# Kernel tuning notes

Measured on AMD Instinct MI355X. Metric: run time of the kernel, lower is better.

The kernel has to match this reference:

```python
import jax, jax.numpy as jnp
import numpy as np

K = 20  # neighbors per point (module default)


def _knn_idx(x, k):
    # x: [N, d] -> indices of k nearest points (self included, as in torch_cluster.knn)
    d2 = jnp.sum(x * x, axis=-1)
    dist = d2[:, None] + d2[None, :] - 2.0 * (x @ x.T)  # [N, N] squared distances
    _, idx = jax.lax.top_k(-dist, k)  # smallest distances
    return idx  # [N, k]


def _mlp(h, layers):
    # layers: list of (W, b, relu_flag); BN is identity (eval mode, fresh running stats)
    for W, b, relu in layers:
        h = h @ W + b
        if relu:
            h = jax.nn.relu(h)
    return h


def _dynamic_edge_conv(x, layers, k=K):
    # x: [B, N, d]; dynamic kNN graph per graph, edge feat [x_i, x_j - x_i], MLP, max-aggr
    idx = jax.vmap(lambda xx: _knn_idx(jax.lax.stop_gradient(xx), k))(x)  # [B, N, k]
    xj = jax.vmap(lambda xx, ii: xx[ii])(x, idx)  # [B, N, k, d] neighbor gather
    xi = x[:, :, None, :]
    feat = jnp.concatenate([jnp.broadcast_to(xi, xj.shape), xj - xi], axis=-1)  # [B,N,k,2d]
    return jnp.max(_mlp(feat, layers), axis=2)  # [B, N, d_out]


def setup_inputs() -> dict:
    key = jax.random.key(0)
    ks = jax.random.split(key, 20)
    s = 0.05
    B, N, PD, OUT = 8, 4096, 2, 10
    f32 = jnp.float32

    def w(k, shape):
        return jax.random.normal(k, shape, dtype=f32) * s

    return {
        "data": jax.random.normal(ks[0], (B, N, PD), dtype=f32),
        # conv1 MLP: [2*PD, 64, 64, 64]
        "c1w1": w(ks[1], (2 * PD, 64)), "c1b1": jnp.zeros((64,), f32),
        "c1w2": w(ks[2], (64, 64)),     "c1b2": jnp.zeros((64,), f32),
        "c1w3": w(ks[3], (64, 64)),     "c1b3": jnp.zeros((64,), f32),
        # conv2 MLP: [2*64, 128]
        "c2w1": w(ks[4], (128, 128)),   "c2b1": jnp.zeros((128,), f32),
        # lin1: 192 -> 1024
        "lin1_w": w(ks[5], (192, 1024)), "lin1_b": jnp.zeros((1024,), f32),
        # head MLP: [1024, 512, 256, OUT]
        "mw1": w(ks[6], (1024, 512)), "mb1": jnp.zeros((512,), f32),
        "mw2": w(ks[7], (512, 256)),  "mb2": jnp.zeros((256,), f32),
        "mw3": w(ks[8], (256, OUT)),  "mb3": jnp.zeros((OUT,), f32),
    }


def reference(data, c1w1, c1b1, c1w2, c1b2, c1w3, c1b3, c2w1, c2b1,
              lin1_w, lin1_b, mw1, mb1, mw2, mb2, mw3, mb3):
    # DynamicEdgeConv 1: MLP([4,64,64,64]) (plain last layer)
    x1 = _dynamic_edge_conv(data, [(c1w1, c1b1, True), (c1w2, c1b2, True), (c1w3, c1b3, False)])
    # DynamicEdgeConv 2: MLP([128,128]) (single plain linear)
    x2 = _dynamic_edge_conv(x1, [(c2w1, c2b1, False)])
    out = jnp.concatenate([x1, x2], axis=-1) @ lin1_w + lin1_b  # [B, N, 1024]
    out = jnp.max(out, axis=1)  # global max pool over points -> [B, 1024]
    out = _mlp(out, [(mw1, mb1, True), (mw2, mb2, True), (mw3, mb3, False)])
    return jax.nn.log_softmax(out, axis=1)
```

## Files before the change

### kernel.cpp

```cpp
#include <hip/hip_runtime.h>
#include <math.h>

#define DEVI static __device__ __forceinline__
#define F_INF __builtin_inff()

typedef short bf16x8 __attribute__((ext_vector_type(8)));
typedef float floatx4 __attribute__((ext_vector_type(4)));
typedef unsigned short ub16x4 __attribute__((ext_vector_type(4)));

DEVI unsigned short bf16rne(float f)
{
    unsigned u = __float_as_uint(f);
    unsigned r = (u + 0x7FFFu + ((u >> 16) & 1u)) >> 16;
    return (unsigned short)r;
}
DEVI float bf16tof(unsigned short h) { return __uint_as_float(((unsigned)h) << 16); }

DEVI bool lexlt(float d, int i, float dr, int ir)
{
    return (d < dr) || (d == dr && i < ir);
}

DEVI void insert20(float* bd, int* bi, float d, int i)
{
#pragma unroll
    for (int j = 19; j >= 1; --j) {
        bool lt  = d < bd[j];
        bool ltp = d < bd[j - 1];
        float nd = ltp ? bd[j - 1] : d;
        int   ni = ltp ? bi[j - 1] : i;
        bd[j] = lt ? nd : bd[j];
        bi[j] = lt ? ni : bi[j];
    }
    bool lt0 = d < bd[0];
    bd[0] = lt0 ? d : bd[0];
    bi[0] = lt0 ? i : bi[0];
}

DEVI void insert_tiered(float* bd, int* bi, float d, int i)
{
    if (__all(!(d < bd[15]))) {
#pragma unroll
        for (int j = 19; j >= 17; --j) {
            bool lt  = d < bd[j];
            bool ltp = d < bd[j - 1];
            float nd = ltp ? bd[j - 1] : d;
            int   ni = ltp ? bi[j - 1] : i;
            bd[j] = lt ? nd : bd[j];
            bi[j] = lt ? ni : bi[j];
        }
        bool lt16 = d < bd[16];
        bd[16] = lt16 ? d : bd[16];
        bi[16] = lt16 ? i : bi[16];
    } else if (__all(!(d < bd[7]))) {
#pragma unroll
        for (int j = 19; j >= 9; --j) {
            bool lt  = d < bd[j];
            bool ltp = d < bd[j - 1];
            float nd = ltp ? bd[j - 1] : d;
            int   ni = ltp ? bi[j - 1] : i;
            bd[j] = lt ? nd : bd[j];
            bi[j] = lt ? ni : bi[j];
        }
        bool lt8 = d < bd[8];
        bd[8] = lt8 ? d : bd[8];
        bi[8] = lt8 ? i : bi[8];
    } else {
        insert20(bd, bi, d, i);
    }
}

DEVI void flushT(float* bd, int* bi, float d, int i, int e, int cnt)
{
    bool want = (e < cnt) && (d < bd[19]);
    if (__any(want))
        insert_tiered(bd, bi, want ? d : F_INF, want ? i : 0x7FFFFFFF);
}

#define FLUSH() do { \
    flushT(bd, bi, a0, j0, 0, cnt); \
    flushT(bd, bi, a1, j1, 1, cnt); \
    flushT(bd, bi, a2, j2, 2, cnt); \
    flushT(bd, bi, a3, j3, 3, cnt); \
    cnt = 0; thr = bd[19]; \
} while (0)

#define APPEND(dv, civ) do { \
    bool pass_ = (dv) < thr; \
    if (pass_) { \
        a0 = (cnt == 0) ? (dv) : a0; j0 = (cnt == 0) ? (civ) : j0; \
        a1 = (cnt == 1) ? (dv) : a1; j1 = (cnt == 1) ? (civ) : j1; \
        a2 = (cnt == 2) ? (dv) : a2; j2 = (cnt == 2) ? (civ) : j2; \
        a3 = (cnt == 3) ? (dv) : a3; j3 = (cnt == 3) ? (civ) : j3; \
        ++cnt; \
    } \
    if (__any(cnt == 4)) { FLUSH(); } \
} while (0)

__global__ __launch_bounds__(64) void k_merge8(const float* __restrict__ partD,
                                               const int* __restrict__ partI,
                                               int* __restrict__ idxo)
{
    int q = blockIdx.x * 64 + threadIdx.x;
    const float* rd = partD + (size_t)q * 160;
    const int*   ri = partI + (size_t)q * 160;
    int p0 = 0, p1 = 0, p2 = 0, p3 = 0, p4 = 0, p5 = 0, p6 = 0, p7 = 0;
    int* op = idxo + (size_t)q * 20;
    for (int r = 0; r < 20; ++r) {
        float d0 = rd[p0],        d1 = rd[20 + p1];
        float d2v = rd[40 + p2],  d3 = rd[60 + p3];
        float d4 = rd[80 + p4],   d5 = rd[100 + p5];
        float d6 = rd[120 + p6],  d7 = rd[140 + p7];
        int   i0 = ri[p0],        i1 = ri[20 + p1];
        int   i2 = ri[40 + p2],   i3 = ri[60 + p3];
        int   i4v = ri[80 + p4],  i5 = ri[100 + p5];
        int   i6 = ri[120 + p6],  i7 = ri[140 + p7];
        bool wA = lexlt(d1, i1, d0, i0);   float dA = wA ? d1 : d0; int iA = wA ? i1 : i0; int sA = wA ? 1 : 0;
        bool wB = lexlt(d3, i3, d2v, i2);  float dB = wB ? d3 : d2v; int iB = wB ? i3 : i2; int sB = wB ? 3 : 2;
        bool wC = lexlt(d5, i5, d4, i4v);  float dC = wC ? d5 : d4; int iC = wC ? i5 : i4v; int sC = wC ? 5 : 4;
        bool wD = lexlt(d7, i7, d6, i6);   float dD = wD ? d7 : d6; int iD = wD ? i7 : i6; int sD = wD ? 7 : 6;
        bool wE = lexlt(dB, iB, dA, iA);   float dE = wE ? dB : dA; int iE = wE ? iB : iA; int sE = wE ? sB : sA;
        bool wF = lexlt(dD, iD, dC, iC);   float dF = wF ? dD : dC; int iF = wF ? iD : iC; int sF = wF ? sD : sC;
        bool wG = lexlt(dF, iF, dE, iE);   int ig = wG ? iF : iE;   int sg = wG ? sF : sE;
        op[r] = ig;
        p0 += (sg == 0); p1 += (sg == 1); p2 += (sg == 2); p3 += (sg == 3);
        p4 += (sg == 4); p5 += (sg == 5); p6 += (sg == 6); p7 += (sg == 7);
    }
}

__global__ __launch_bounds__(256, 4) void k_knn2d(const float* __restrict__ x,
                                                  float* __restrict__ partD, int* __restrict__ partI)
{
    __shared__ float2 pts[4096];
    int t = threadIdx.x;
    int blk = blockIdx.x;
    int b = blk >> 7;
    int qt = (blk >> 1) & 63;
    int s = blk & 1;
    const float* xb = x + (size_t)b * 4096 * 2;
    for (int f = t; f < 2048; f += 256)
        ((float4*)pts)[f] = ((const float4*)xb)[f];
    __syncthreads();

    int l = t & 63, w = t >> 6;
    int q = qt * 64 + l;
    float2 qp = pts[q];
    float d2i = qp.x * qp.x + qp.y * qp.y;

    float bd[20]; int bi[20];
#pragma unroll
    for (int j = 0; j < 20; ++j) { bd[j] = F_INF; bi[j] = -1; }
    int cnt = 0; float thr = F_INF;
    float a0 = 0, a1 = 0, a2 = 0, a3 = 0;
    int   j0 = 0, j1 = 0, j2 = 0, j3 = 0;

    int m0 = s * 2048 + w * 512;
    for (int m = m0; m < m0 + 512; ++m) {
        float2 p = pts[m];
        float d2j = p.x * p.x + p.y * p.y;
        float dot = qp.x * p.x + qp.y * p.y;
        float dist = (d2i + d2j) - 2.0f * dot;
        APPEND(dist, m);
    }
    FLUSH();

    size_t base = (((size_t)(b * 4096 + q)) * 8 + s * 4 + w) * 20;
#pragma unroll
    for (int k = 0; k < 20; ++k) { partD[base + k] = bd[k]; partI[base + k] = bi[k]; }
}

__global__ void k_prep1(const float* __restrict__ x, const float* __restrict__ w1,
                        const float* __restrict__ b1, float* __restrict__ pm, float* __restrict__ qv)
{
    int tid = blockIdx.x * 256 + threadIdx.x;
    int n = tid >> 6, i = tid & 63;
    float x0 = x[(size_t)n * 2], x1v = x[(size_t)n * 2 + 1];
    float wa = w1[i], wb = w1[64 + i], wc = w1[128 + i], wd = w1[192 + i];
    pm[tid] = fmaf(x0, wa - wc, fmaf(x1v, wb - wd, b1[i]));
    qv[tid] = fmaf(x0, wc, x1v * wd);
}

__global__ __launch_bounds__(256) void k_edge1(const float* __restrict__ pm, const float* __restrict__ q,
                                               const int* __restrict__ idx1,
                                               const float* __restrict__ w2, const float* __restrict__ b2,
                                               const float* __restrict__ w3, const float* __restrict__ b3,
                                               float* __restrict__ x1, float* __restrict__ d2x1)
{
    int t = threadIdx.x;
    int w = t >> 6, l = t & 63;
    int pg = l / 20;
    int k  = l - pg * 20;
    int n0 = blockIdx.x * 12 + w * 3 + pg;
    bool valid = (l < 60) && (n0 < 32768);
    int n = valid ? n0 : 0;
    int b = n >> 12;
    int j = idx1[(size_t)n * 20 + k];
    const float4* pmr = (const float4*)(pm + (size_t)n * 64);
    const float4* qr  = (const float4*)(q + ((size_t)(b * 4096) + j) * 64);

    float h1[64];
#pragma unroll
    for (int i4 = 0; i4 < 16; ++i4) {
        float4 a = pmr[i4], c = qr[i4];
        h1[i4 * 4 + 0] = fmaxf(a.x + c.x, 0.f);
        h1[i4 * 4 + 1] = fmaxf(a.y + c.y, 0.f);
        h1[i4 * 4 + 2] = fmaxf(a.z + c.z, 0.f);
        h1[i4 * 4 + 3] = fmaxf(a.w + c.w, 0.f);
    }
    float h2[64];
#pragma unroll
    for (int o = 0; o < 64; ++o) h2[o] = b2[o];
#pragma unroll
    for (int i = 0; i < 64; ++i) {
        const float* r = w2 + i * 64;
#pragma unroll
        for (int o = 0; o < 64; ++o) h2[o] = fmaf(h1[i], r[o], h2[o]);
    }
#pragma unroll
    for (int o = 0; o < 64; ++o) h2[o] = fmaxf(h2[o], 0.f);

    float h3[64];
#pragma unroll
    for (int o = 0; o < 64; ++o) h3[o] = b3[o];
#pragma unroll
    for (int i = 0; i < 64; ++i) {
        const float* r = w3 + i * 64;
#pragma unroll
        for (int o = 0; o < 64; ++o) h3[o] = fmaf(h2[i], r[o], h3[o]);
    }

    int s16 = (k + 16 < 20) ? (l + 16) : l;
    int s8  = (k + 8  < 20) ? (l + 8)  : l;
    int s4  = (k + 4  < 20) ? (l + 4)  : l;
    int s2  = (k + 2  < 20) ? (l + 2)  : l;
    int s1  = (k + 1  < 20) ? (l + 1)  : l;
#pragma unroll
    for (int o = 0; o < 64; ++o) {
        float v = h3[o];
        v = fmaxf(v, __shfl(v, s16));
        v = fmaxf(v, __shfl(v, s8));
        v = fmaxf(v, __shfl(v, s4));
        v = fmaxf(v, __shfl(v, s2));
        v = fmaxf(v, __shfl(v, s1));
        h3[o] = v;
    }
    if (valid && k == 0) {
        float d2 = 0.f;
#pragma unroll
        for (int o = 0; o < 64; ++o) d2 += h3[o] * h3[o];
        float4* op = (float4*)(x1 + (size_t)n * 64);
#pragma unroll
        for (int i4 = 0; i4 < 16; ++i4)
            op[i4] = make_float4(h3[i4 * 4], h3[i4 * 4 + 1], h3[i4 * 4 + 2], h3[i4 * 4 + 3]);
        d2x1[n] = d2;
    }
}

__global__ __launch_bounds__(256) void k_split(const float* __restrict__ x1,
                                               unsigned short* __restrict__ xh,
                                               unsigned short* __restrict__ xm,
                                               unsigned short* __restrict__ xl)
{
    int id = blockIdx.x * 256 + threadIdx.x;
    float4 v = ((const float4*)x1)[id];
    float vv[4] = { v.x, v.y, v.z, v.w };
    ub16x4 h, m, l;
#pragma unroll
    for (int i = 0; i < 4; ++i) {
        float x = vv[i];
        unsigned short hb = bf16rne(x);  float fh = bf16tof(hb);
        float r1 = x - fh;
        unsigned short mb = bf16rne(r1); float fm = bf16tof(mb);
        float r2 = r1 - fm;
        unsigned short lb = bf16rne(r2);
        h[i] = hb; m[i] = mb; l[i] = lb;
    }
    ((ub16x4*)xh)[id] = h;
    ((ub16x4*)xm)[id] = m;
    ((ub16x4*)xl)[id] = l;
}

__global__ __launch_bounds__(256, 3) void k_knn64(const unsigned short* __restrict__ xh,
                                                  const unsigned short* __restrict__ xm,
                                                  const unsigned short* __restrict__ xl,
                                                  const float* __restrict__ d2x1,
                                                  float* __restrict__ partD, int* __restrict__ partI)
{
    __shared__ unsigned short qlds[1536 * 8];
    __shared__ float dlds[4 * 16 * 68];
    __shared__ float d2cL[64];

    int t = threadIdx.x;
    int blk = blockIdx.x;
    int bb = blk >> 7;
    int qt = (blk >> 1) & 63;
    int s  = blk & 1;
    int qbase  = bb * 4096 + qt * 64;
    int cstart = s * 2048;
    int w = t >> 6, l = t & 63;
    int r16 = l & 15, g = l >> 4;

    {
        const unsigned short* pp[3] = { xh, xm, xl };
        for (int f = t; f < 1536; f += 256) {
            int lane = f & 63, kc = (f >> 6) & 1, qb = (f >> 7) & 3, pl = f >> 9;
            size_t off = ((size_t)(qbase + qb * 16 + (lane & 15))) * 64 + kc * 32 + 8 * (lane >> 4);
            ((bf16x8*)qlds)[f] = *(const bf16x8*)(pp[pl] + off);
        }
    }
    float d2ql = d2x1[qbase + l];
    __syncthreads();

    float bd[20]; int bi[20];
#pragma unroll
    for (int j = 0; j < 20; ++j) { bd[j] = F_INF; bi[j] = -1; }
    int cnt = 0; float thr = F_INF;
    float a0 = 0, a1 = 0, a2 = 0, a3 = 0;
    int   j0 = 0, j1 = 0, j2 = 0, j3 = 0;

    const bf16x8* qf = (const bf16x8*)qlds;
    float* myD = dlds + w * 16 * 68;

    for (int T = 0; T < 32; ++T) {
        int csl = cstart + T * 64 + 16 * w;
        int csg = bb * 4096 + csl;

        bf16x8 bh[2], bm[2], blv[2];
#pragma unroll
        for (int kc = 0; kc < 2; ++kc) {
            size_t off = ((size_t)(csg + r16)) * 64 + kc * 32 + 8 * g;
            bh[kc]  = *(const bf16x8*)(xh + off);
            bm[kc]  = *(const bf16x8*)(xm + off);
            blv[kc] = *(const bf16x8*)(xl + off);
        }
        if (l < 16) d2cL[w * 16 + l] = d2x1[csg + l];

        floatx4 acc[4];
#pragma unroll
        for (int qb = 0; qb < 4; ++qb) acc[qb] = (floatx4){0.f, 0.f, 0.f, 0.f};
#pragma unroll
        for (int qb = 0; qb < 4; ++qb)
#pragma unroll
            for (int kc = 0; kc < 2; ++kc) {
                bf16x8 qh_ = qf[((0 * 4 + qb) * 2 + kc) * 64 + l];
                bf16x8 qm_ = qf[((1 * 4 + qb) * 2 + kc) * 64 + l];
                bf16x8 ql_ = qf[((2 * 4 + qb) * 2 + kc) * 64 + l];
                acc[qb] = __builtin_amdgcn_mfma_f32_16x16x32_bf16(qh_, bh[kc],  acc[qb], 0, 0, 0);
                acc[qb] = __builtin_amdgcn_mfma_f32_16x16x32_bf16(qh_, bm[kc],  acc[qb], 0, 0, 0);
                acc[qb] = __builtin_amdgcn_mfma_f32_16x16x32_bf16(qm_, bh[kc],  acc[qb], 0, 0, 0);
                acc[qb] = __builtin_amdgcn_mfma_f32_16x16x32_bf16(qm_, bm[kc],  acc[qb], 0, 0, 0);
                acc[qb] = __builtin_amdgcn_mfma_f32_16x16x32_bf16(qh_, blv[kc], acc[qb], 0, 0, 0);
                acc[qb] = __builtin_amdgcn_mfma_f32_16x16x32_bf16(ql_, bh[kc],  acc[qb], 0, 0, 0);
            }

#pragma unroll
        for (int qb = 0; qb < 4; ++qb)
#pragma unroll
            for (int rr = 0; rr < 4; ++rr)
                myD[r16 * 68 + qb * 16 + g * 4 + rr] = acc[qb][rr];

#pragma unroll
        for (int c = 0; c < 16; ++c) {
            float dot = myD[c * 68 + l];
            float dist = (d2ql + d2cL[w * 16 + c]) - 2.0f * dot;
            APPEND(dist, csl + c);
        }
    }
    FLUSH();

    size_t base = (((size_t)(qbase + l)) * 8 + s * 4 + w) * 20;
#pragma unroll
    for (int k = 0; k < 20; ++k) { partD[base + k] = bd[k]; partI[base + k] = bi[k]; }
}

__global__ __launch_bounds__(128) void k_prep2(const float* __restrict__ x1, const float* __restrict__ w,
                                               const float* __restrict__ bias,
                                               float* __restrict__ T, float* __restrict__ V)
{
    __shared__ float xs[8][64];
    int o = threadIdx.x;
    int g = blockIdx.x * 8;
    for (int t = threadIdx.x; t < 512; t += 128) xs[t >> 6][t & 63] = x1[(size_t)g * 64 + t];
    __syncthreads();
    float at[8] = {}, av[8] = {};
    for (int i = 0; i < 64; ++i) {
        float wt = w[i * 128 + o], wv = w[(64 + i) * 128 + o];
#pragma unroll
        for (int p = 0; p < 8; ++p) {
            float xv = xs[p][i];
            at[p] = fmaf(xv, wt, at[p]);
            av[p] = fmaf(xv, wv, av[p]);
        }
    }
    float bo = bias[o];
#pragma unroll
    for (int p = 0; p < 8; ++p) {
        T[(size_t)(g + p) * 128 + o] = at[p] - av[p] + bo;
        V[(size_t)(g + p) * 128 + o] = av[p];
    }
}

__global__ __launch_bounds__(256) void k_edge2(const float* __restrict__ T, const float* __restrict__ V,
                                               const int* __restrict__ idx2, float* __restrict__ x2)
{
    int t = threadIdx.x;
    int p = t >> 5, oc = t & 31;
    int n = blockIdx.x * 8 + p;
    int b = n >> 12;
    const int* ip = idx2 + (size_t)n * 20;
    float4 mx = make_float4(-F_INF, -F_INF, -F_INF, -F_INF);
    for (int k = 0; k < 20; ++k) {
        int j = ip[k];
        float4 v = ((const float4*)(V + ((size_t)(b * 4096) + j) * 128))[oc];
        mx.x = fmaxf(mx.x, v.x); mx.y = fmaxf(mx.y, v.y);
        mx.z = fmaxf(mx.z, v.z); mx.w = fmaxf(mx.w, v.w);
    }
    float4 tv = ((const float4*)(T + (size_t)n * 128))[oc];
    float4 r = make_float4(tv.x + mx.x, tv.y + mx.y, tv.z + mx.z, tv.w + mx.w);
    ((float4*)(x2 + (size_t)n * 128))[oc] = r;
}

__global__ __launch_bounds__(256) void k_lin1max(const float* __restrict__ x1, const float* __restrict__ x2,
                                                 const float* __restrict__ w, const float* __restrict__ bias,
                                                 float* __restrict__ partial)
{
    __shared__ float fs[32][192];
    int blk = blockIdx.x;
    int b = blk >> 7, c = blk & 127;
    int base_n = b * 4096 + c * 32;
    for (int t = threadIdx.x; t < 2048; t += 256) {
        int n = t >> 6, i = t & 63;
        fs[n][i] = x1[(size_t)(base_n + n) * 64 + i];
    }
    for (int t = threadIdx.x; t < 4096; t += 256) {
        int n = t >> 7, i = t & 127;
        fs[n][64 + i] = x2[(size_t)(base_n + n) * 128 + i];
    }
    __syncthreads();

    float acc[32][4];
#pragma unroll
    for (int n = 0; n < 32; ++n)
#pragma unroll
        for (int oo = 0; oo < 4; ++oo) acc[n][oo] = 0.f;

    for (int i4 = 0; i4 < 48; ++i4) {
        float wv[4][4];
#pragma unroll
        for (int r = 0; r < 4; ++r)
#pragma unroll
            for (int oo = 0; oo < 4; ++oo)
                wv[r][oo] = w[(size_t)(i4 * 4 + r) * 1024 + oo * 256 + threadIdx.x];
#pragma unroll
        for (int n = 0; n < 32; ++n) {
            float4 f = *(const float4*)&fs[n][i4 * 4];
#pragma unroll
            for (int oo = 0; oo < 4; ++oo) {
                acc[n][oo] = fmaf(f.x, wv[0][oo], acc[n][oo]);
                acc[n][oo] = fmaf(f.y, wv[1][oo], acc[n][oo]);
                acc[n][oo] = fmaf(f.z, wv[2][oo], acc[n][oo]);
                acc[n][oo] = fmaf(f.w, wv[3][oo], acc[n][oo]);
            }
        }
    }
#pragma unroll
    for (int oo = 0; oo < 4; ++oo) {
        int o = oo * 256 + threadIdx.x;
        float m = -F_INF;
#pragma unroll
        for (int n = 0; n < 32; ++n) m = fmaxf(m, acc[n][oo]);
        partial[((size_t)b * 128 + c) * 1024 + o] = m + bias[o];
    }
}

__global__ void k_red(const float* __restrict__ partial, float* __restrict__ pooled)
{
    int t = blockIdx.x * 256 + threadIdx.x;
    int b = t >> 10, o = t & 1023;
    float m = -F_INF;
    for (int c = 0; c < 128; ++c) m = fmaxf(m, partial[((size_t)b * 128 + c) * 1024 + o]);
    pooled[t] = m;
}

__global__ __launch_bounds__(256) void k_fc1(const float* __restrict__ pooled, const float* __restrict__ w,
                                             const float* __restrict__ bias, float* __restrict__ g1)
{
    __shared__ float ps[8 * 1024];
    for (int t = threadIdx.x; t < 8192; t += 256) ps[t] = pooled[t];
    __syncthreads();
    int o = blockIdx.x * 256 + threadIdx.x;
    float acc[8] = {};
    for (int i4 = 0; i4 < 256; ++i4) {
        float w0 = w[(size_t)(i4 * 4 + 0) * 512 + o];
        float w1v = w[(size_t)(i4 * 4 + 1) * 512 + o];
        float w2v = w[(size_t)(i4 * 4 + 2) * 512 + o];
        float w3v = w[(size_t)(i4 * 4 + 3) * 512 + o];
#pragma unroll
        for (int bb = 0; bb < 8; ++bb) {
            float4 f = *(const float4*)&ps[bb * 1024 + i4 * 4];
            acc[bb] = fmaf(f.x, w0, fmaf(f.y, w1v, fmaf(f.z, w2v, fmaf(f.w, w3v, acc[bb]))));
        }
    }
    float bo = bias[o];
#pragma unroll
    for (int bb = 0; bb < 8; ++bb) g1[bb * 512 + o] = fmaxf(acc[bb] + bo, 0.f);
}

__global__ __launch_bounds__(256) void k_fc2(const float* __restrict__ g1, const float* __restrict__ w,
                                             const float* __restrict__ bias, float* __restrict__ g2)
{
    __shared__ float gs[8 * 512];
    for (int t = threadIdx.x; t < 4096; t += 256) gs[t] = g1[t];
    __syncthreads();
    int o = threadIdx.x;
    float acc[8] = {};
    for (int i4 = 0; i4 < 128; ++i4) {
        float w0 = w[(size_t)(i4 * 4 + 0) * 256 + o];
        float w1v = w[(size_t)(i4 * 4 + 1) * 256 + o];
        float w2v = w[(size_t)(i4 * 4 + 2) * 256 + o];
        float w3v = w[(size_t)(i4 * 4 + 3) * 256 + o];
#pragma unroll
        for (int bb = 0; bb < 8; ++bb) {
            float4 f = *(const float4*)&gs[bb * 512 + i4 * 4];
            acc[bb] = fmaf(f.x, w0, fmaf(f.y, w1v, fmaf(f.z, w2v, fmaf(f.w, w3v, acc[bb]))));
        }
    }
    float bo = bias[o];
#pragma unroll
    for (int bb = 0; bb < 8; ++bb) g2[bb * 256 + o] = fmaxf(acc[bb] + bo, 0.f);
}

__global__ void k_fc3sm(const float* __restrict__ g2, const float* __restrict__ w,
                        const float* __restrict__ bias, float* __restrict__ out)
{
    int t = threadIdx.x;
    int b = t >> 4, l = t & 15;
    float lg = -F_INF;
    if (l < 10) {
        float a = bias[l];
        for (int i = 0; i < 256; ++i) a = fmaf(g2[b * 256 + i], w[i * 10 + l], a);
        lg = a;
    }
    float m = lg;
    m = fmaxf(m, __shfl_xor(m, 1, 16));
    m = fmaxf(m, __shfl_xor(m, 2, 16));
    m = fmaxf(m, __shfl_xor(m, 4, 16));
    m = fmaxf(m, __shfl_xor(m, 8, 16));
    float e = (l < 10) ? expf(lg - m) : 0.f;
    float s = e;
    s += __shfl_xor(s, 1, 16);
    s += __shfl_xor(s, 2, 16);
    s += __shfl_xor(s, 4, 16);
    s += __shfl_xor(s, 8, 16);
    if (l < 10) out[b * 10 + l] = (lg - m) - logf(s);
}

extern "C" void kernel_launch(void* const* d_in, const int* in_sizes, int n_in,
                              void* d_out, int out_size, void* d_ws, size_t ws_size,
                              hipStream_t stream)
{
    (void)in_sizes; (void)n_in; (void)out_size; (void)ws_size;
    const float* data  = (const float*)d_in[0];
    const float* c1w1  = (const float*)d_in[1];
    const float* c1b1  = (const float*)d_in[2];
    const float* c1w2  = (const float*)d_in[3];
    const float* c1b2  = (const float*)d_in[4];
    const float* c1w3  = (const float*)d_in[5];
    const float* c1b3  = (const float*)d_in[6];
    const float* c2w1  = (const float*)d_in[7];
    const float* c2b1  = (const float*)d_in[8];
    const float* lin1w = (const float*)d_in[9];
    const float* lin1b = (const float*)d_in[10];
    const float* mw1   = (const float*)d_in[11];
    const float* mb1   = (const float*)d_in[12];
    const float* mw2   = (const float*)d_in[13];
    const float* mb2   = (const float*)d_in[14];
    const float* mw3   = (const float*)d_in[15];
    const float* mb3   = (const float*)d_in[16];
    float* ws  = (float*)d_ws;
    int*   wsi = (int*)d_ws;
    float* out = (float*)d_out;

    const size_t OFF_IDX1 = 0;
    const size_t OFF_IDX2 = 0;
    const size_t OFF_X1   = 655360;
    const size_t OFF_D2   = 2752512;
    const size_t OFF_PM   = 2785280;
    const size_t OFF_Q    = 4882432;
    const size_t OFF_PD   = 2785280;
    const size_t OFF_PI   = 8028160;
    const size_t OFF_T    = 2785280;
    const size_t OFF_V    = 6979584;
    const size_t OFF_X2   = 11173888;
    const size_t OFF_PART = 15368192;
    const size_t OFF_POOL = 16416768;
    const size_t OFF_G1   = 16424960;
    const size_t OFF_G2   = 16429056;
    const size_t OFF_XH   = 13271040;
    const size_t OFF_XM   = 14319616;
    const size_t OFF_XL   = 15368192;

    k_knn2d<<<1024, 256, 0, stream>>>(data, ws + OFF_PD, wsi + OFF_PI);
    k_merge8<<<512, 64, 0, stream>>>(ws + OFF_PD, wsi + OFF_PI, wsi + OFF_IDX1);
    k_prep1<<<8192, 256, 0, stream>>>(data, c1w1, c1b1, ws + OFF_PM, ws + OFF_Q);
    k_edge1<<<2731, 256, 0, stream>>>(ws + OFF_PM, ws + OFF_Q, wsi + OFF_IDX1,
                                      c1w2, c1b2, c1w3, c1b3, ws + OFF_X1, ws + OFF_D2);
    k_split<<<2048, 256, 0, stream>>>(ws + OFF_X1,
                                      (unsigned short*)(ws + OFF_XH),
                                      (unsigned short*)(ws + OFF_XM),
                                      (unsigned short*)(ws + OFF_XL));
    k_knn64<<<1024, 256, 0, stream>>>((const unsigned short*)(ws + OFF_XH),
                                      (const unsigned short*)(ws + OFF_XM),
                                      (const unsigned short*)(ws + OFF_XL),
                                      ws + OFF_D2, ws + OFF_PD, wsi + OFF_PI);
    k_merge8<<<512, 64, 0, stream>>>(ws + OFF_PD, wsi + OFF_PI, wsi + OFF_IDX2);
    k_prep2<<<4096, 128, 0, stream>>>(ws + OFF_X1, c2w1, c2b1, ws + OFF_T, ws + OFF_V);
    k_edge2<<<4096, 256, 0, stream>>>(ws + OFF_T, ws + OFF_V, wsi + OFF_IDX2, ws + OFF_X2);
    k_lin1max<<<1024, 256, 0, stream>>>(ws + OFF_X1, ws + OFF_X2, lin1w, lin1b, ws + OFF_PART);
    k_red<<<32, 256, 0, stream>>>(ws + OFF_PART, ws + OFF_POOL);
    k_fc1<<<2, 256, 0, stream>>>(ws + OFF_POOL, mw1, mb1, ws + OFF_G1);
    k_fc2<<<1, 256, 0, stream>>>(ws + OFF_G1, mw2, mb2, ws + OFF_G2);
    k_fc3sm<<<1, 128, 0, stream>>>(ws + OFF_G2, mw3, mb3, out);
}
```

Baseline: 1.663 ms.

## Interleave bf16 split planes, transpose partial top-k layout, reorder knn64 block mapping

Packs the three bf16 split planes (hi/mid/lo) of each point into one interleaved 192-element row, so each candidate's three fragments share cache lines. Changes the partial top-k buffers from per-query-contiguous to per-slice-major, so lanes in a wavefront write and read adjacent query records in the knn and merge kernels. Remaps k_knn64 block indices so consecutive blocks cover different batches with the same query tile, and adds a __syncthreads at the top of each candidate tile loop, which looks like a fix for an LDS reuse race. The extra barrier adds some synchronisation cost per tile.

```diff
diff --git a/kernel.cpp b/kernel.cpp
--- a/kernel.cpp
+++ b/kernel.cpp
@@ -101,20 +101,21 @@
                                                const int* __restrict__ partI,
                                                int* __restrict__ idxo)
 {
+    const size_t LS = 655360;
     int q = blockIdx.x * 64 + threadIdx.x;
-    const float* rd = partD + (size_t)q * 160;
-    const int*   ri = partI + (size_t)q * 160;
+    const float* rd = partD + (size_t)q * 20;
+    const int*   ri = partI + (size_t)q * 20;
     int p0 = 0, p1 = 0, p2 = 0, p3 = 0, p4 = 0, p5 = 0, p6 = 0, p7 = 0;
     int* op = idxo + (size_t)q * 20;
     for (int r = 0; r < 20; ++r) {
-        float d0 = rd[p0],        d1 = rd[20 + p1];
-        float d2v = rd[40 + p2],  d3 = rd[60 + p3];
-        float d4 = rd[80 + p4],   d5 = rd[100 + p5];
-        float d6 = rd[120 + p6],  d7 = rd[140 + p7];
-        int   i0 = ri[p0],        i1 = ri[20 + p1];
-        int   i2 = ri[40 + p2],   i3 = ri[60 + p3];
-        int   i4v = ri[80 + p4],  i5 = ri[100 + p5];
-        int   i6 = ri[120 + p6],  i7 = ri[140 + p7];
+        float d0 = rd[p0],            d1 = rd[LS + p1];
+        float d2v = rd[2 * LS + p2],  d3 = rd[3 * LS + p3];
+        float d4 = rd[4 * LS + p4],   d5 = rd[5 * LS + p5];
+        float d6 = rd[6 * LS + p6],   d7 = rd[7 * LS + p7];
+        int   i0 = ri[p0],            i1 = ri[LS + p1];
+        int   i2 = ri[2 * LS + p2],   i3 = ri[3 * LS + p3];
+        int   i4v = ri[4 * LS + p4],  i5 = ri[5 * LS + p5];
+        int   i6 = ri[6 * LS + p6],   i7 = ri[7 * LS + p7];
         bool wA = lexlt(d1, i1, d0, i0);   float dA = wA ? d1 : d0; int iA = wA ? i1 : i0; int sA = wA ? 1 : 0;
         bool wB = lexlt(d3, i3, d2v, i2);  float dB = wB ? d3 : d2v; int iB = wB ? i3 : i2; int sB = wB ? 3 : 2;
         bool wC = lexlt(d5, i5, d4, i4v);  float dC = wC ? d5 : d4; int iC = wC ? i5 : i4v; int sC = wC ? 5 : 4;
@@ -164,7 +165,7 @@
     }
     FLUSH();
 
-    size_t base = (((size_t)(b * 4096 + q)) * 8 + s * 4 + w) * 20;
+    size_t base = (((size_t)(s * 4 + w)) * 32768 + (b * 4096 + q)) * 20;
 #pragma unroll
     for (int k = 0; k < 20; ++k) { partD[base + k] = bd[k]; partI[base + k] = bi[k]; }
 }
@@ -257,11 +258,10 @@
 }
 
 __global__ __launch_bounds__(256) void k_split(const float* __restrict__ x1,
-                                               unsigned short* __restrict__ xh,
-                                               unsigned short* __restrict__ xm,
-                                               unsigned short* __restrict__ xl)
+                                               unsigned short* __restrict__ xi)
 {
     int id = blockIdx.x * 256 + threadIdx.x;
+    int n = id >> 4, dp = id & 15;
     float4 v = ((const float4*)x1)[id];
     float vv[4] = { v.x, v.y, v.z, v.w };
     ub16x4 h, m, l;
@@ -275,14 +275,13 @@
         unsigned short lb = bf16rne(r2);
         h[i] = hb; m[i] = mb; l[i] = lb;
     }
-    ((ub16x4*)xh)[id] = h;
-    ((ub16x4*)xm)[id] = m;
-    ((ub16x4*)xl)[id] = l;
-}
-
-__global__ __launch_bounds__(256, 3) void k_knn64(const unsigned short* __restrict__ xh,
-                                                  const unsigned short* __restrict__ xm,
-                                                  const unsigned short* __restrict__ xl,
+    size_t rb = (size_t)n * 192;
+    *(ub16x4*)(xi + rb +       dp * 4) = h;
+    *(ub16x4*)(xi + rb +  64 + dp * 4) = m;
+    *(ub16x4*)(xi + rb + 128 + dp * 4) = l;
+}
+
+__global__ __launch_bounds__(256, 3) void k_knn64(const unsigned short* __restrict__ xi,
                                                   const float* __restrict__ d2x1,
                                                   float* __restrict__ partD, int* __restrict__ partI)
 {
@@ -292,21 +291,19 @@
 
     int t = threadIdx.x;
     int blk = blockIdx.x;
-    int bb = blk >> 7;
-    int qt = (blk >> 1) & 63;
+    int qt = blk >> 4;
+    int bb = (blk >> 1) & 7;
     int s  = blk & 1;
     int qbase  = bb * 4096 + qt * 64;
     int cstart = s * 2048;
     int w = t >> 6, l = t & 63;
     int r16 = l & 15, g = l >> 4;
 
-    {
-        const unsigned short* pp[3] = { xh, xm, xl };
-        for (int f = t; f < 1536; f += 256) {
-            int lane = f & 63, kc = (f >> 6) & 1, qb = (f >> 7) & 3, pl = f >> 9;
-            size_t off = ((size_t)(qbase + qb * 16 + (lane & 15))) * 64 + kc * 32 + 8 * (lane >> 4);
-            ((bf16x8*)qlds)[f] = *(const bf16x8*)(pp[pl] + off);
-        }
+    for (int f = t; f < 1536; f += 256) {
+        int lane = f & 63, kc = (f >> 6) & 1, qb = (f >> 7) & 3, pl = f >> 9;
+        size_t off = ((size_t)(qbase + qb * 16 + (lane & 15))) * 192 + pl * 64
+                   + kc * 32 + 8 * (lane >> 4);
+        ((bf16x8*)qlds)[f] = *(const bf16x8*)(xi + off);
     }
     float d2ql = d2x1[qbase + l];
     __syncthreads();
@@ -322,16 +319,17 @@
     float* myD = dlds + w * 16 * 68;
 
     for (int T = 0; T < 32; ++T) {
+        __syncthreads();
         int csl = cstart + T * 64 + 16 * w;
         int csg = bb * 4096 + csl;
 
         bf16x8 bh[2], bm[2], blv[2];
 #pragma unroll
         for (int kc = 0; kc < 2; ++kc) {
-            size_t off = ((size_t)(csg + r16)) * 64 + kc * 32 + 8 * g;
-            bh[kc]  = *(const bf16x8*)(xh + off);
-            bm[kc]  = *(const bf16x8*)(xm + off);
-            blv[kc] = *(const bf16x8*)(xl + off);
+            size_t rb = ((size_t)(csg + r16)) * 192 + kc * 32 + 8 * g;
+            bh[kc]  = *(const bf16x8*)(xi + rb);
+            bm[kc]  = *(const bf16x8*)(xi + rb + 64);
+            blv[kc] = *(const bf16x8*)(xi + rb + 128);
         }
         if (l < 16) d2cL[w * 16 + l] = d2x1[csg + l];
 
@@ -368,7 +366,7 @@
     }
     FLUSH();
 
-    size_t base = (((size_t)(qbase + l)) * 8 + s * 4 + w) * 20;
+    size_t base = (((size_t)(s * 4 + w)) * 32768 + (qbase + l)) * 20;
 #pragma unroll
     for (int k = 0; k < 20; ++k) { partD[base + k] = bd[k]; partI[base + k] = bi[k]; }
 }
@@ -596,22 +594,15 @@
     const size_t OFF_POOL = 16416768;
     const size_t OFF_G1   = 16424960;
     const size_t OFF_G2   = 16429056;
-    const size_t OFF_XH   = 13271040;
-    const size_t OFF_XM   = 14319616;
-    const size_t OFF_XL   = 15368192;
+    const size_t OFF_XI   = 13271040;
 
     k_knn2d<<<1024, 256, 0, stream>>>(data, ws + OFF_PD, wsi + OFF_PI);
     k_merge8<<<512, 64, 0, stream>>>(ws + OFF_PD, wsi + OFF_PI, wsi + OFF_IDX1);
     k_prep1<<<8192, 256, 0, stream>>>(data, c1w1, c1b1, ws + OFF_PM, ws + OFF_Q);
     k_edge1<<<2731, 256, 0, stream>>>(ws + OFF_PM, ws + OFF_Q, wsi + OFF_IDX1,
                                       c1w2, c1b2, c1w3, c1b3, ws + OFF_X1, ws + OFF_D2);
-    k_split<<<2048, 256, 0, stream>>>(ws + OFF_X1,
-                                      (unsigned short*)(ws + OFF_XH),
-                                      (unsigned short*)(ws + OFF_XM),
-                                      (unsigned short*)(ws + OFF_XL));
-    k_knn64<<<1024, 256, 0, stream>>>((const unsigned short*)(ws + OFF_XH),
-                                      (const unsigned short*)(ws + OFF_XM),
-                                      (const unsigned short*)(ws + OFF_XL),
+    k_split<<<2048, 256, 0, stream>>>(ws + OFF_X1, (unsigned short*)(ws + OFF_XI));
+    k_knn64<<<1024, 256, 0, stream>>>((const unsigned short*)(ws + OFF_XI),
                                       ws + OFF_D2, ws + OFF_PD, wsi + OFF_PI);
     k_merge8<<<512, 64, 0, stream>>>(ws + OFF_PD, wsi + OFF_PI, wsi + OFF_IDX2);
     k_prep2<<<4096, 128, 0, stream>>>(ws + OFF_X1, c2w1, c2b1, ws + OFF_T, ws + OFF_V);
```

New measurement: 1.456 ms. -12.4%, faster.
